# Performance work log

Measured on AMD Instinct MI355X. Metric: run time of the kernel, lower is better.

## Reference

```python
import jax, jax.numpy as jnp
import numpy as np

B, S, D = 2, 2048, 1024
E, H = 8, 2816  # hidden = 256*ceil(int(2*(4*1024)/3)/256) = 2816
TOP_K = 2


def setup_inputs() -> dict:
    key = jax.random.key(0)
    k0, k1, k2, k3, k4 = jax.random.split(key, 5)
    x = jax.random.normal(k0, (B, S, D), dtype=jnp.float32)
    wg = jax.random.normal(k1, (D, E), dtype=jnp.float32) * (D ** -0.5)
    w1 = jax.random.normal(k2, (E, D, H), dtype=jnp.float32) * 0.02  # gate proj
    w3 = jax.random.normal(k3, (E, D, H), dtype=jnp.float32) * 0.02  # up proj
    w2 = jax.random.normal(k4, (E, H, D), dtype=jnp.float32) * 0.02  # down proj
    return {"x": x, "wg": wg, "w1": w1, "w2": w2, "w3": w3}


def reference(x, wg, w1, w2, w3):
    Bb, Ss, Dd = x.shape
    Ee = w1.shape[0]
    xf = x.reshape(-1, Dd)                       # [T, D]
    logits = xf @ wg                              # [T, E]
    probs = jax.nn.softmax(logits, axis=-1)
    topk_p, topk_i = jax.lax.top_k(probs, TOP_K)  # [T, K]
    topk_p = topk_p / jnp.sum(topk_p, axis=-1, keepdims=True)
    # combine weight per (token, expert): sum over top-k slots
    cw = jnp.sum(jax.nn.one_hot(topk_i, Ee, dtype=xf.dtype) * topk_p[..., None], axis=1)  # [T, E]
    out = jnp.zeros_like(xf)
    for e in range(Ee):  # fixed small loop over experts
        h = jax.nn.silu(xf @ w1[e]) * (xf @ w3[e])   # [T, H] SwiGLU
        out = out + cw[:, e:e + 1] * (h @ w2[e])     # weighted combine
    return out.reshape(Bb, Ss, Dd)
```

## Files before the change

kernel.cpp:

```cpp
#include <hip/hip_runtime.h>
#include <hip/hip_bf16.h>

typedef unsigned short u16;
typedef __bf16 bf16_t;
typedef bf16_t bf16x8 __attribute__((ext_vector_type(8)));
typedef float f32x4 __attribute__((ext_vector_type(4)));

#define T_TOK 4096
#define DIM   1024
#define NEXP  8
#define HID   2816
#define CAP   16

static __device__ __forceinline__ u16 f2b(float f) {
    __hip_bfloat16 h = __float2bfloat16(f);
    return *(u16*)&h;
}

static __device__ __forceinline__ void glds16(const u16* g, u16* l) {
    __builtin_amdgcn_global_load_lds((const __attribute__((address_space(1))) void*)g,
                                     (__attribute__((address_space(3))) void*)l, 16, 0, 0);
}

__global__ void k_gating(const float* __restrict__ X,
                         const float* __restrict__ WG,
                         int* __restrict__ cnt,
                         int* __restrict__ tok,
                         float* __restrict__ wt,
                         u16* __restrict__ Xbf)
{
    int wv   = threadIdx.x >> 6;
    int lane = threadIdx.x & 63;
    int t = blockIdx.x * 4 + wv;
    float l[NEXP];
#pragma unroll
    for (int e = 0; e < NEXP; ++e) l[e] = 0.f;
#pragma unroll
    for (int i = 0; i < DIM/64; ++i) {
        int d = i*64 + lane;
        float xv = X[(size_t)t*DIM + d];
        Xbf[(size_t)t*DIM + d] = f2b(xv);
        const float* wrow = WG + (size_t)d*NEXP;
        float4 wa = *(const float4*)wrow;
        float4 wb = *(const float4*)(wrow + 4);
        l[0] += xv*wa.x; l[1] += xv*wa.y; l[2] += xv*wa.z; l[3] += xv*wa.w;
        l[4] += xv*wb.x; l[5] += xv*wb.y; l[6] += xv*wb.z; l[7] += xv*wb.w;
    }
#pragma unroll
    for (int e = 0; e < NEXP; ++e) {
#pragma unroll
        for (int s = 32; s > 0; s >>= 1)
            l[e] += __shfl_xor(l[e], s, 64);
    }
    if (lane == 0) {
        int i1 = 0; float b1 = l[0];
#pragma unroll
        for (int e = 1; e < NEXP; ++e) if (l[e] > b1) { b1 = l[e]; i1 = e; }
        int i2 = -1; float b2 = 0.f;
#pragma unroll
        for (int e = 0; e < NEXP; ++e) {
            if (e == i1) continue;
            if (i2 < 0 || l[e] > b2) { b2 = l[e]; i2 = e; }
        }
        float p1 = 1.f / (1.f + __expf(b2 - b1));
        float p2 = 1.f - p1;
        int pos = atomicAdd(&cnt[i1], 1);
        tok[i1*T_TOK + pos] = t;  wt[i1*T_TOK + pos] = p1;
        pos = atomicAdd(&cnt[i2], 1);
        tok[i2*T_TOK + pos] = t;  wt[i2*T_TOK + pos] = p2;
    }
}

__global__ void k_compact(const int* __restrict__ cnt,
                          const int* __restrict__ tok, const float* __restrict__ wt,
                          int* __restrict__ ctok, float* __restrict__ cwt)
{
    int e = blockIdx.x;
    int off = 0;
    for (int i = 0; i < e; ++i) off += cnt[i];
    int n = cnt[e];
    for (int i = threadIdx.x; i < n; i += blockDim.x) {
        ctok[off + i] = tok[e*T_TOK + i];
        cwt [off + i] = wt [e*T_TOK + i];
    }
}

#define TS 72
__global__ void k_transpose_cast(const float* __restrict__ in, u16* __restrict__ out,
                                 int R, int C)
{
    __shared__ u16 tle[64*TS];
    size_t mb = (size_t)blockIdx.z * (size_t)R * C;
    int r0 = blockIdx.x * 64, c0 = blockIdx.y * 64;
    int tid = threadIdx.x;
    const float* I = in + mb + (size_t)r0*C + c0;
#pragma unroll
    for (int p = 0; p < 4; ++p) {
        int q = tid + p*256;
        int r = q >> 4, cc = (q & 15) * 4;
        float4 v = *(const float4*)&I[(size_t)r*C + cc];
        tle[(cc+0)*TS + r] = f2b(v.x);
        tle[(cc+1)*TS + r] = f2b(v.y);
        tle[(cc+2)*TS + r] = f2b(v.z);
        tle[(cc+3)*TS + r] = f2b(v.w);
    }
    __syncthreads();
    u16* O = out + mb + (size_t)c0*R + r0;
    int rc = tid & 7, oc = tid >> 3;
#pragma unroll
    for (int p = 0; p < 2; ++p) {
        int c = oc + p*32;
        *(uint4*)&O[(size_t)c*R + rc*8] = *(const uint4*)&tle[c*TS + rc*8];
    }
}

__global__ __launch_bounds__(256, 3) void k_gemm1(
    const u16* __restrict__ X, const u16* __restrict__ W1t, const u16* __restrict__ W3t,
    u16* __restrict__ Hbuf, const int* __restrict__ cnt, const int* __restrict__ ctok)
{
    __shared__ u16 As[128*32];
    __shared__ u16 Bs[128*32];
    __shared__ int tokLds[128];

    const int bid = blockIdx.x;
    const int e   = bid & 7;
    const int q   = bid >> 3;
    const int mt0 = q & (CAP-1);
    const int col = q >> 4;
    const int ne  = cnt[e];
    const int ntile = (ne + 127) >> 7;
    if (mt0 >= ntile) return;
    int off = 0;
    for (int i = 0; i < e; ++i) off += cnt[i];
    const int h0 = col * 64;

    const int tid = threadIdx.x, wave = tid >> 6, lane = tid & 63;
    const int wr = wave >> 1, wc = wave & 1;
    const int quad = lane >> 4, lr = lane & 15;
    const int lrow = lane >> 2;
    const int swk  = ((lane & 3) ^ ((lane >> 3) & 3)) * 8;
    const int jx   = (quad ^ ((lr >> 1) & 3)) * 8;

    const size_t wb = (size_t)e * HID * DIM;
    const u16* w1g = W1t + wb + (size_t)(h0 + wave*16 + lrow)*DIM + swk;
    const u16* w3g = W3t + wb + (size_t)(h0 + wave*16 + lrow)*DIM + swk;
    u16* aL0 = &As[(wave*16)*32];
    u16* aL1 = &As[(64 + wave*16)*32];
    u16* bL0 = &Bs[(wave*16)*32];
    u16* bL1 = &Bs[(64 + wave*16)*32];

    for (int tile = mt0; tile < ntile; tile += CAP) {
        const int m0 = tile << 7;
        int nvalid = ne - m0; if (nvalid > 128) nvalid = 128;

        __syncthreads();
        if (tid < 128) {
            int i = (tid < nvalid) ? tid : (nvalid - 1);
            tokLds[tid] = ctok[off + m0 + i];
        }
        __syncthreads();
        const u16* ag0 = X + (size_t)tokLds[wave*16 + lrow]*DIM + swk;
        const u16* ag1 = X + (size_t)tokLds[64 + wave*16 + lrow]*DIM + swk;

        f32x4 a1[4][2], a3[4][2];
#pragma unroll
        for (int m = 0; m < 4; ++m)
#pragma unroll
            for (int n = 0; n < 2; ++n) {
                a1[m][n] = (f32x4){0.f,0.f,0.f,0.f};
                a3[m][n] = (f32x4){0.f,0.f,0.f,0.f};
            }

        for (int k0 = 0; k0 < DIM; k0 += 32) {
            __syncthreads();
            glds16(ag0 + k0, aL0);
            glds16(ag1 + k0, aL1);
            glds16(w1g + k0, bL0);
            glds16(w3g + k0, bL1);
            __syncthreads();
            bf16x8 af[4], b1[2], b3[2];
#pragma unroll
            for (int m = 0; m < 4; ++m)
                af[m] = *(const bf16x8*)&As[(wr*64 + m*16 + lr)*32 + jx];
#pragma unroll
            for (int n = 0; n < 2; ++n) {
                b1[n] = *(const bf16x8*)&Bs[(wc*32 + n*16 + lr)*32 + jx];
                b3[n] = *(const bf16x8*)&Bs[(64 + wc*32 + n*16 + lr)*32 + jx];
            }
#pragma unroll
            for (int m = 0; m < 4; ++m)
#pragma unroll
                for (int n = 0; n < 2; ++n) {
                    a1[m][n] = __builtin_amdgcn_mfma_f32_16x16x32_bf16(af[m], b1[n], a1[m][n], 0, 0, 0);
                    a3[m][n] = __builtin_amdgcn_mfma_f32_16x16x32_bf16(af[m], b3[n], a3[m][n], 0, 0, 0);
                }
        }

#pragma unroll
        for (int m = 0; m < 4; ++m) {
            int mb_ = wr*64 + m*16 + quad*4;
#pragma unroll
            for (int rr = 0; rr < 4; ++rr) {
                int mm = mb_ + rr;
                if (mm >= nvalid) continue;
                u16* hrow = Hbuf + (size_t)(off + m0 + mm)*HID + h0 + wc*32 + lr;
#pragma unroll
                for (int n = 0; n < 2; ++n) {
                    float g = a1[m][n][rr];
                    float u = a3[m][n][rr];
                    hrow[n*16] = f2b((g / (1.f + __expf(-g))) * u);
                }
            }
        }
    }
}

__global__ __launch_bounds__(256, 3) void k_gemm2(
    const u16* __restrict__ Hbuf, const u16* __restrict__ W2t,
    float* __restrict__ outf, const int* __restrict__ cnt,
    const int* __restrict__ ctok, const float* __restrict__ cwt)
{
    __shared__ u16 As[128*32];
    __shared__ u16 Bs[128*32];
    __shared__ int   tLds[128];
    __shared__ float wLds[128];

    const int bid = blockIdx.x;
    const int e   = bid & 7;
    const int q   = bid >> 3;
    const int mt0 = q & (CAP-1);
    const int r2  = q >> 4;
    const int zk  = r2 & 1;
    const int d0  = (r2 >> 1) * 128;
    const int ne  = cnt[e];
    const int ntile = (ne + 127) >> 7;
    if (mt0 >= ntile) return;
    int off = 0;
    for (int i = 0; i < e; ++i) off += cnt[i];
    const int kb = zk * (HID/2);

    const int tid = threadIdx.x, wave = tid >> 6, lane = tid & 63;
    const int wr = wave >> 1, wc = wave & 1;
    const int quad = lane >> 4, lr = lane & 15;
    const int lrow = lane >> 2;
    const int swk  = ((lane & 3) ^ ((lane >> 3) & 3)) * 8;
    const int jx   = (quad ^ ((lr >> 1) & 3)) * 8;

    const size_t w2b = (size_t)e * DIM * HID;
    const u16* bg0 = W2t + w2b + (size_t)(d0 + wave*16 + lrow)*HID + kb + swk;
    const u16* bg1 = bg0 + (size_t)64*HID;
    u16* aL0 = &As[(wave*16)*32];
    u16* aL1 = &As[(64 + wave*16)*32];
    u16* bL0 = &Bs[(wave*16)*32];
    u16* bL1 = &Bs[(64 + wave*16)*32];

    for (int tile = mt0; tile < ntile; tile += CAP) {
        const int m0 = tile << 7;
        int nvalid = ne - m0; if (nvalid > 128) nvalid = 128;

        __syncthreads();
        if (tid < 128) {
            int i = (tid < nvalid) ? tid : (nvalid - 1);
            tLds[tid] = ctok[off + m0 + i];
            wLds[tid] = cwt [off + m0 + i];
        }
        __syncthreads();
        int ar0 = wave*16 + lrow;      if (ar0 >= nvalid) ar0 = nvalid - 1;
        int ar1 = 64 + wave*16 + lrow; if (ar1 >= nvalid) ar1 = nvalid - 1;
        const u16* ag0 = Hbuf + (size_t)(off + m0 + ar0)*HID + kb + swk;
        const u16* ag1 = Hbuf + (size_t)(off + m0 + ar1)*HID + kb + swk;

        f32x4 acc[4][4];
#pragma unroll
        for (int a = 0; a < 4; ++a)
#pragma unroll
            for (int b = 0; b < 4; ++b) acc[a][b] = (f32x4){0.f,0.f,0.f,0.f};

        for (int k0 = 0; k0 < HID/2; k0 += 32) {
            __syncthreads();
            glds16(ag0 + k0, aL0);
            glds16(ag1 + k0, aL1);
            glds16(bg0 + k0, bL0);
            glds16(bg1 + k0, bL1);
            __syncthreads();
            bf16x8 af[4], bf[4];
#pragma unroll
            for (int m = 0; m < 4; ++m)
                af[m] = *(const bf16x8*)&As[(wr*64 + m*16 + lr)*32 + jx];
#pragma unroll
            for (int n = 0; n < 4; ++n)
                bf[n] = *(const bf16x8*)&Bs[(wc*64 + n*16 + lr)*32 + jx];
#pragma unroll
            for (int m = 0; m < 4; ++m)
#pragma unroll
                for (int n = 0; n < 4; ++n)
                    acc[m][n] = __builtin_amdgcn_mfma_f32_16x16x32_bf16(af[m], bf[n], acc[m][n], 0, 0, 0);
        }

#pragma unroll
        for (int m = 0; m < 4; ++m) {
            int mb_ = wr*64 + m*16 + quad*4;
#pragma unroll
            for (int rr = 0; rr < 4; ++rr) {
                int mm = mb_ + rr;
                if (mm >= nvalid) continue;
                float wr_ = wLds[mm];
                float* orow = outf + (size_t)tLds[mm]*DIM + d0 + wc*64 + lr;
#pragma unroll
                for (int n = 0; n < 4; ++n)
                    atomicAdd(&orow[n*16], acc[m][n][rr] * wr_);
            }
        }
    }
}

extern "C" void kernel_launch(void* const* d_in, const int* in_sizes, int n_in,
                              void* d_out, int out_size, void* d_ws, size_t ws_size,
                              hipStream_t stream)
{
    const float* x  = (const float*)d_in[0];
    const float* wg = (const float*)d_in[1];
    const float* w1 = (const float*)d_in[2];
    const float* w2 = (const float*)d_in[3];
    const float* w3 = (const float*)d_in[4];
    float* outf = (float*)d_out;

    char* ws = (char*)d_ws;
    int*   cnt  = (int*)  (ws);
    int*   tok  = (int*)  (ws + 256);
    float* wt   = (float*)(ws + 131328);
    int*   ctok = (int*)  (ws + 262400);
    float* cwt  = (float*)(ws + 295168);
    u16*   Xbf  = (u16*)  (ws + 327936);
    u16*   Hbuf = (u16*)  (ws + 8716544);
    u16*   W1t  = (u16*)  (ws + 54853888);
    u16*   W3t  = (u16*)  (ws + 100991232);
    u16*   W2t  = (u16*)  (ws + 147128576);

    hipMemsetAsync(cnt, 0, 256, stream);
    hipMemsetAsync(outf, 0, (size_t)T_TOK*DIM*sizeof(float), stream);

    k_transpose_cast<<<dim3(DIM/64, HID/64, NEXP), 256, 0, stream>>>(w1, W1t, DIM, HID);
    k_transpose_cast<<<dim3(DIM/64, HID/64, NEXP), 256, 0, stream>>>(w3, W3t, DIM, HID);
    k_transpose_cast<<<dim3(HID/64, DIM/64, NEXP), 256, 0, stream>>>(w2, W2t, HID, DIM);

    k_gating<<<T_TOK/4, 256, 0, stream>>>(x, wg, cnt, tok, wt, Xbf);
    k_compact<<<NEXP, 256, 0, stream>>>(cnt, tok, wt, ctok, cwt);

    k_gemm1<<<NEXP*(HID/64)*CAP, 256, 0, stream>>>(Xbf, W1t, W3t, Hbuf, cnt, ctok);
    k_gemm2<<<NEXP*CAP*2*(DIM/128), 256, 0, stream>>>(Hbuf, W2t, outf, cnt, ctok, cwt);
}
```

Baseline: 663.1 us.

## Double-buffer LDS tiles and prefetch next K-slice in both expert GEMMs

Both grouped GEMM kernels now use two LDS buffers: the next 32-wide K slice is issued via global_load_lds while MFMAs consume the current one. Synchronisation uses explicit vmcnt/lgkmcnt waits and raw barriers, and MFMA sections raise wave priority. This aims to hide global load latency that previously stalled each iteration behind two __syncthreads. It doubles LDS use per block, which may limit occupancy, and relies on hand-written wait counts.

After: 663.8 us. About the same (+0.1%).

```diff
diff --git a/kernel.cpp b/kernel.cpp
--- a/kernel.cpp
+++ b/kernel.cpp
@@ -11,6 +11,7 @@
 #define NEXP  8
 #define HID   2816
 #define CAP   16
+#define DBUF  (128*32)
 
 static __device__ __forceinline__ u16 f2b(float f) {
     __hip_bfloat16 h = __float2bfloat16(f);
@@ -118,8 +119,8 @@
     const u16* __restrict__ X, const u16* __restrict__ W1t, const u16* __restrict__ W3t,
     u16* __restrict__ Hbuf, const int* __restrict__ cnt, const int* __restrict__ ctok)
 {
-    __shared__ u16 As[128*32];
-    __shared__ u16 Bs[128*32];
+    __shared__ u16 As[2*DBUF];
+    __shared__ u16 Bs[2*DBUF];
     __shared__ int tokLds[128];
 
     const int bid = blockIdx.x;
@@ -149,6 +150,34 @@
     u16* bL0 = &Bs[(wave*16)*32];
     u16* bL1 = &Bs[(64 + wave*16)*32];
 
+#define G1_STAGE(K, OFS)              \
+    glds16(ag0 + (K), aL0 + (OFS));   \
+    glds16(ag1 + (K), aL1 + (OFS));   \
+    glds16(w1g + (K), bL0 + (OFS));   \
+    glds16(w3g + (K), bL1 + (OFS));
+
+#define G1_COMPUTE(OFS)                                                             \
+    {                                                                               \
+        bf16x8 af[4], b1[2], b3[2];                                                 \
+        _Pragma("unroll")                                                           \
+        for (int m = 0; m < 4; ++m)                                                 \
+            af[m] = *(const bf16x8*)&As[(OFS) + (wr*64 + m*16 + lr)*32 + jx];       \
+        _Pragma("unroll")                                                           \
+        for (int n = 0; n < 2; ++n) {                                               \
+            b1[n] = *(const bf16x8*)&Bs[(OFS) + (wc*32 + n*16 + lr)*32 + jx];       \
+            b3[n] = *(const bf16x8*)&Bs[(OFS) + (64 + wc*32 + n*16 + lr)*32 + jx];  \
+        }                                                                           \
+        __builtin_amdgcn_s_setprio(1);                                              \
+        _Pragma("unroll")                                                           \
+        for (int m = 0; m < 4; ++m)                                                 \
+            _Pragma("unroll")                                                       \
+            for (int n = 0; n < 2; ++n) {                                           \
+                a1[m][n] = __builtin_amdgcn_mfma_f32_16x16x32_bf16(af[m], b1[n], a1[m][n], 0, 0, 0); \
+                a3[m][n] = __builtin_amdgcn_mfma_f32_16x16x32_bf16(af[m], b3[n], a3[m][n], 0, 0, 0); \
+            }                                                                       \
+        __builtin_amdgcn_s_setprio(0);                                              \
+    }
+
     for (int tile = mt0; tile < ntile; tile += CAP) {
         const int m0 = tile << 7;
         int nvalid = ne - m0; if (nvalid > 128) nvalid = 128;
@@ -171,29 +200,25 @@
                 a3[m][n] = (f32x4){0.f,0.f,0.f,0.f};
             }
 
-        for (int k0 = 0; k0 < DIM; k0 += 32) {
-            __syncthreads();
-            glds16(ag0 + k0, aL0);
-            glds16(ag1 + k0, aL1);
-            glds16(w1g + k0, bL0);
-            glds16(w3g + k0, bL1);
-            __syncthreads();
-            bf16x8 af[4], b1[2], b3[2];
-#pragma unroll
-            for (int m = 0; m < 4; ++m)
-                af[m] = *(const bf16x8*)&As[(wr*64 + m*16 + lr)*32 + jx];
-#pragma unroll
-            for (int n = 0; n < 2; ++n) {
-                b1[n] = *(const bf16x8*)&Bs[(wc*32 + n*16 + lr)*32 + jx];
-                b3[n] = *(const bf16x8*)&Bs[(64 + wc*32 + n*16 + lr)*32 + jx];
+        G1_STAGE(0, 0)
+
+        for (int k0 = 0; k0 < DIM; k0 += 64) {
+            G1_STAGE(k0 + 32, DBUF)
+            asm volatile("s_waitcnt vmcnt(4)" ::: "memory");
+            __builtin_amdgcn_s_barrier();
+            G1_COMPUTE(0)
+            asm volatile("s_waitcnt lgkmcnt(0)" ::: "memory");
+            __builtin_amdgcn_s_barrier();
+            if (k0 + 64 < DIM) {
+                G1_STAGE(k0 + 64, 0)
+                asm volatile("s_waitcnt vmcnt(4)" ::: "memory");
+            } else {
+                asm volatile("s_waitcnt vmcnt(0)" ::: "memory");
             }
-#pragma unroll
-            for (int m = 0; m < 4; ++m)
-#pragma unroll
-                for (int n = 0; n < 2; ++n) {
-                    a1[m][n] = __builtin_amdgcn_mfma_f32_16x16x32_bf16(af[m], b1[n], a1[m][n], 0, 0, 0);
-                    a3[m][n] = __builtin_amdgcn_mfma_f32_16x16x32_bf16(af[m], b3[n], a3[m][n], 0, 0, 0);
-                }
+            __builtin_amdgcn_s_barrier();
+            G1_COMPUTE(DBUF)
+            asm volatile("s_waitcnt lgkmcnt(0)" ::: "memory");
+            __builtin_amdgcn_s_barrier();
         }
 
 #pragma unroll
@@ -213,6 +238,8 @@
             }
         }
     }
+#undef G1_STAGE
+#undef G1_COMPUTE
 }
 
 __global__ __launch_bounds__(256, 3) void k_gemm2(
@@ -220,8 +247,8 @@
     float* __restrict__ outf, const int* __restrict__ cnt,
     const int* __restrict__ ctok, const float* __restrict__ cwt)
 {
-    __shared__ u16 As[128*32];
-    __shared__ u16 Bs[128*32];
+    __shared__ u16 As[2*DBUF];
+    __shared__ u16 Bs[2*DBUF];
     __shared__ int   tLds[128];
     __shared__ float wLds[128];
 
@@ -254,6 +281,30 @@
     u16* bL0 = &Bs[(wave*16)*32];
     u16* bL1 = &Bs[(64 + wave*16)*32];
 
+#define G2_STAGE(K, OFS)              \
+    glds16(ag0 + (K), aL0 + (OFS));   \
+    glds16(ag1 + (K), aL1 + (OFS));   \
+    glds16(bg0 + (K), bL0 + (OFS));   \
+    glds16(bg1 + (K), bL1 + (OFS));
+
+#define G2_COMPUTE(OFS)                                                             \
+    {                                                                               \
+        bf16x8 af[4], bb[4];                                                        \
+        _Pragma("unroll")                                                           \
+        for (int m = 0; m < 4; ++m)                                                 \
+            af[m] = *(const bf16x8*)&As[(OFS) + (wr*64 + m*16 + lr)*32 + jx];       \
+        _Pragma("unroll")                                                           \
+        for (int n = 0; n < 4; ++n)                                                 \
+            bb[n] = *(const bf16x8*)&Bs[(OFS) + (wc*64 + n*16 + lr)*32 + jx];       \
+        __builtin_amdgcn_s_setprio(1);                                              \
+        _Pragma("unroll")                                                           \
+        for (int m = 0; m < 4; ++m)                                                 \
+            _Pragma("unroll")                                                       \
+            for (int n = 0; n < 4; ++n)                                             \
+                acc[m][n] = __builtin_amdgcn_mfma_f32_16x16x32_bf16(af[m], bb[n], acc[m][n], 0, 0, 0); \
+        __builtin_amdgcn_s_setprio(0);                                              \
+    }
+
     for (int tile = mt0; tile < ntile; tile += CAP) {
         const int m0 = tile << 7;
         int nvalid = ne - m0; if (nvalid > 128) nvalid = 128;
@@ -276,25 +327,25 @@
 #pragma unroll
             for (int b = 0; b < 4; ++b) acc[a][b] = (f32x4){0.f,0.f,0.f,0.f};
 
-        for (int k0 = 0; k0 < HID/2; k0 += 32) {
-            __syncthreads();
-            glds16(ag0 + k0, aL0);
-            glds16(ag1 + k0, aL1);
-            glds16(bg0 + k0, bL0);
-            glds16(bg1 + k0, bL1);
-            __syncthreads();
-            bf16x8 af[4], bf[4];
-#pragma unroll
-            for (int m = 0; m < 4; ++m)
-                af[m] = *(const bf16x8*)&As[(wr*64 + m*16 + lr)*32 + jx];
-#pragma unroll
-            for (int n = 0; n < 4; ++n)
-                bf[n] = *(const bf16x8*)&Bs[(wc*64 + n*16 + lr)*32 + jx];
-#pragma unroll
-            for (int m = 0; m < 4; ++m)
-#pragma unroll
-                for (int n = 0; n < 4; ++n)
-                    acc[m][n] = __builtin_amdgcn_mfma_f32_16x16x32_bf16(af[m], bf[n], acc[m][n], 0, 0, 0);
+        G2_STAGE(0, 0)
+
+        for (int k0 = 0; k0 < HID/2; k0 += 64) {
+            G2_STAGE(k0 + 32, DBUF)
+            asm volatile("s_waitcnt vmcnt(4)" ::: "memory");
+            __builtin_amdgcn_s_barrier();
+            G2_COMPUTE(0)
+            asm volatile("s_waitcnt lgkmcnt(0)" ::: "memory");
+            __builtin_amdgcn_s_barrier();
+            if (k0 + 64 < HID/2) {
+                G2_STAGE(k0 + 64, 0)
+                asm volatile("s_waitcnt vmcnt(4)" ::: "memory");
+            } else {
+                asm volatile("s_waitcnt vmcnt(0)" ::: "memory");
+            }
+            __builtin_amdgcn_s_barrier();
+            G2_COMPUTE(DBUF)
+            asm volatile("s_waitcnt lgkmcnt(0)" ::: "memory");
+            __builtin_amdgcn_s_barrier();
         }
 
 #pragma unroll
@@ -312,6 +363,8 @@
             }
         }
     }
+#undef G2_STAGE
+#undef G2_COMPUTE
 }
 
 extern "C" void kernel_launch(void* const* d_in, const int* in_sizes, int n_in,
```
